# Kernel tuning notes

Hardware: AMD Instinct MI355X
Metric: run time of the kernel (lower is better)

Reference implementation:

```python
import jax, jax.numpy as jnp
import numpy as np

KEEP_FRAC = 0.8
HOP_CLIP = 15000  # reached hops are tiny; clip so score fits int32


def _bfs_keep_mask(src, dst, perm, n_nodes):
    """Replicates do_augmentation: BFS hop via u_add_e/min message passing,
    with a tie-break that seeds one unreached node when the frontier stalls,
    then keeps the 80% closest nodes (ties broken by perm)."""
    root = perm[0]
    w = jnp.where(src == dst, 0.0, 1.0).astype(jnp.float32)  # self-loop weight 0
    hop0 = jnp.full((n_nodes,), float(n_nodes), jnp.float32).at[root].set(0.0)
    thresh = n_nodes - 0.5
    cnt_target = int(n_nodes * KEEP_FRAC)

    def cond(state):
        return state[1] <= cnt_target

    def body(state):
        hop, cnt, hc = state
        m = jax.ops.segment_min(hop[src] + w, dst, num_segments=n_nodes)
        hop = jnp.minimum(m, hop)  # min-reduce (self-loops keep hop monotone)
        hc = hc + 1
        new_cnt = jnp.sum(hop < thresh).astype(jnp.int32)
        stuck = new_cnt == cnt
        # pick an unreached node (random in original; perm-ordered here)
        idx = jnp.argmin(jnp.where(hop > thresh, perm, 2 * n_nodes))
        hop = jnp.where(stuck, hop.at[idx].set(hc.astype(jnp.float32)), hop)
        new_cnt = new_cnt + stuck.astype(jnp.int32)
        return hop, new_cnt, hc

    cnt0 = jnp.sum(hop0 < thresh).astype(jnp.int32)
    hop, _, _ = jax.lax.while_loop(cond, body, (hop0, cnt0, jnp.int32(0)))
    score = jnp.minimum(hop, HOP_CLIP).astype(jnp.int32) * n_nodes + perm
    order = jnp.argsort(score)
    keep = jnp.zeros((n_nodes,), bool).at[order[:cnt_target]].set(True)
    return keep


def _gcn(x, src, dst, edge_mask, W_enc, n_nodes):
    # mean-aggregation GCN layer: h = relu(mean_{in-nbrs} x @ W)
    msg = x[src] * edge_mask[:, None]                      # [E, D]
    agg = jax.ops.segment_sum(msg, dst, num_segments=n_nodes)
    deg = jax.ops.segment_sum(edge_mask, dst, num_segments=n_nodes)
    return jax.nn.relu((agg / jnp.maximum(deg, 1.0)[:, None]) @ W_enc)


def _bce_with_logits(logits, positive):
    # BCEWithLogitsLoss: target=1 -> softplus(-x); target=0 -> softplus(x)
    return jnp.mean(jax.nn.softplus(jnp.where(positive, -logits, logits)))


def reference(feat, W_enc, W_disc, src, dst, perm_neg, perm1, perm2):
    n = feat.shape[0]
    ones_e = jnp.ones(src.shape[0], jnp.float32)
    pos = _gcn(feat, src, dst, ones_e, W_enc, n)           # [N, H]
    neg = _gcn(feat[perm_neg], src, dst, ones_e, W_enc, n)

    k = int(n * KEEP_FRAC)
    total = jnp.float32(0.0)
    for perm in (perm1, perm2):
        keep = _bfs_keep_mask(src, dst, perm, n)
        em = (keep[src] & keep[dst]).astype(jnp.float32)
        h = _gcn(feat * keep[:, None], src, dst, em, W_enc, n)
        summary = jax.nn.sigmoid(jnp.sum(h * keep[:, None], axis=0) / k)
        v = W_disc @ summary                               # [H]
        total = total + _bce_with_logits(pos @ v, True) + _bce_with_logits(neg @ v, False)
    return total


def setup_inputs() -> dict:
    key = jax.random.key(0)
    ks = jax.random.split(key, 8)
    N, D, H, DEG = 100000, 64, 64, 16
    E = N * DEG
    src = jnp.concatenate([jax.random.randint(ks[0], (E,), 0, N, jnp.int32),
                           jnp.arange(N, dtype=jnp.int32)])  # + self-loops
    dst = jnp.concatenate([jax.random.randint(ks[1], (E,), 0, N, jnp.int32),
                           jnp.arange(N, dtype=jnp.int32)])
    feat = jax.random.normal(ks[2], (N, D), jnp.float32)
    W_enc = jax.random.normal(ks[3], (D, H), jnp.float32) * (1.0 / np.sqrt(D))
    bound = 1.0 / np.sqrt(H)
    W_disc = jax.random.uniform(ks[4], (H, H), jnp.float32, -bound, bound)
    perm_neg = jax.random.permutation(ks[5], N).astype(jnp.int32)
    perm1 = jax.random.permutation(ks[6], N).astype(jnp.int32)
    perm2 = jax.random.permutation(ks[7], N).astype(jnp.int32)
    return {"feat": feat, "W_enc": W_enc, "W_disc": W_disc, "src": src,
            "dst": dst, "perm_neg": perm_neg, "perm1": perm1, "perm2": perm2}
```

## Files before the change

kernel.cpp:

```cpp
#include <hip/hip_runtime.h>
#include <hip/hip_fp8.h>
#include <hip/hip_fp16.h>

#define BS 256
#define MAXIT 7
#define UNREACHED 0x3f3f3f3f
#define NR 256
#define RB 256

#define C_DONE  0
#define C_CNT   1
#define C_BLKA  2
#define C_BLKB  3
#define C_BLKC  4
#define C_NEWA  20
#define C_LOSS  32
#define C_V1    192
#define C_V2    256

typedef __hip_fp8_e4m3 fp8;

#define ALr(p)   __hip_atomic_load((p), __ATOMIC_RELAXED, __HIP_MEMORY_SCOPE_AGENT)
#define ALf(p)   __hip_atomic_load((p), __ATOMIC_RELAXED, __HIP_MEMORY_SCOPE_AGENT)
#define ASr(p,v) __hip_atomic_store((p),(v), __ATOMIC_RELAXED, __HIP_MEMORY_SCOPE_AGENT)
#define ASl(p,v) __hip_atomic_store((p),(v), __ATOMIC_RELEASE, __HIP_MEMORY_SCOPE_AGENT)

__device__ inline float softplusf(float x){
  return fmaxf(x, 0.f) + log1pf(expf(-fabsf(x)));
}

__device__ inline void cut_hr(const int* __restrict__ ctl, int target, int& hstar, int& r){
  int c=1;
  hstar=63; r=0;
  for(int h=1;h<=MAXIT;h++){
    int x=ctl[C_NEWA+h-1];
    if(c+x>target){ hstar=h; r=target-c; return; }
    c+=x;
  }
  r=target-c;
}

__global__ void k_rhist(const int* __restrict__ dst, int E, int* __restrict__ hist,
                        int* __restrict__ bktBase, int nbk, int* __restrict__ ctrl){
  __shared__ int lh[512];
  int b=blockIdx.x, t=threadIdx.x;
  for(int i=t;i<nbk;i+=BS) lh[i]=0;
  __syncthreads();
  int per=(E+RB-1)/RB;
  int s0=b*per, s1=min(s0+per,E);
  for(int i=s0+t;i<s1;i+=BS) atomicAdd(&lh[dst[i]>>8],1);
  __syncthreads();
  for(int i=t;i<nbk;i+=BS) hist[i*RB+b]=lh[i];
  __shared__ int isLast;
  __syncthreads();
  if(t==0){
    __threadfence();
    isLast=(atomicAdd(&ctrl[C_BLKA],1)==(int)gridDim.x-1);
  }
  __syncthreads();
  if(!isLast) return;
  __threadfence();
  for(int r=t;r<nbk;r+=BS){
    const int* h=&hist[r*RB];
    int a=0;
    for(int bb=0;bb<RB;bb++) a+=ALr(&h[bb]);
    lh[r]=a;
  }
  __syncthreads();
  if(t==0){
    int acc=0;
    for(int r=0;r<nbk;r++){ bktBase[r]=acc; acc+=lh[r]; }
    bktBase[nbk]=E;
    ASr(&ctrl[C_BLKA],0);
    __threadfence();
  }
}

__global__ void k_cursors(const int* __restrict__ hist, const int* __restrict__ bktBase,
                          int* __restrict__ cursorTab, int nbk){
  __shared__ int s[BS];
  int r=blockIdx.x, t=threadIdx.x;
  if(r>=nbk) return;
  int v=hist[r*RB+t];
  s[t]=v; __syncthreads();
  for(int o=1;o<BS;o<<=1){
    int x=(t>=o)? s[t-o]:0;
    __syncthreads();
    if(t>=o) s[t]+=x;
    __syncthreads();
  }
  cursorTab[r*RB+t]=bktBase[r]+s[t]-v;
}

__global__ void k_rscatter(const int* __restrict__ dst, const int* __restrict__ src, int E,
                           const int* __restrict__ cursorTab,
                           unsigned long long* __restrict__ pairs, int nbk){
  __shared__ int cur[512];
  int b=blockIdx.x, t=threadIdx.x;
  for(int r=t;r<nbk;r+=BS) cur[r]=cursorTab[r*RB+b];
  __syncthreads();
  int per=(E+RB-1)/RB;
  int s0=b*per, s1=min(s0+per,E);
  for(int i=s0+t;i<s1;i+=BS){
    int d=dst[i], s=src[i];
    int pos=atomicAdd(&cur[d>>8],1);
    pairs[pos]=((unsigned long long)(unsigned)d<<32)|(unsigned)s;
  }
}

__global__ void k_bplace2(const int* __restrict__ bktBase, const unsigned long long* __restrict__ pairs,
                          int* __restrict__ rowptr, int* __restrict__ colD, int N, int E){
  __shared__ int cnt[NR];
  __shared__ int s[NR];
  __shared__ int cur[NR];
  int b=blockIdx.x, t=threadIdx.x;
  int v0=b*NR, v1=min(v0+NR,N), nv=v1-v0;
  int s0=bktBase[b], e0=bktBase[b+1];
  cnt[t]=0;
  __syncthreads();
  for(int i=s0+t;i<e0;i+=BS){
    int d=(int)(pairs[i]>>32);
    atomicAdd(&cnt[d-v0],1);
  }
  __syncthreads();
  int v=(t<nv)?cnt[t]:0;
  s[t]=v; __syncthreads();
  for(int o=1;o<BS;o<<=1){
    int x=(t>=o)? s[t-o]:0;
    __syncthreads();
    if(t>=o) s[t]+=x;
    __syncthreads();
  }
  int excl=s[t]-v+s0;
  if(t<nv){ rowptr[v0+t]=excl; cur[t]=excl; }
  if(b==0&&t==0) rowptr[N]=E;
  __syncthreads();
  for(int i=s0+t;i<e0;i+=BS){
    unsigned long long p=pairs[i];
    int d=(int)(p>>32), sv=(int)(p&0xffffffffu);
    int pos=atomicAdd(&cur[d-v0],1);
    colD[pos]=sv;
  }
}

__global__ void k_fw(const float* __restrict__ feat, const float* __restrict__ W,
                     fp8* __restrict__ FWI, int N){
  __shared__ float sW[64*64];
  __shared__ float sf[4][64];
  int t=threadIdx.x;
  for(int i=t;i<64*64;i+=BS) sW[i]=W[i];
  __syncthreads();
  int j=t&63, r=t>>6;
  int ngroups=(N+3)>>2;
  for(int g=blockIdx.x; g<ngroups; g+=gridDim.x){
    int vr=g*4+r;
    sf[r][j] = (vr<N)? feat[vr*64+j] : 0.f;
    __syncthreads();
    if(vr<N){
      float acc=0.f;
      #pragma unroll
      for(int d=0;d<64;d++) acc += sf[r][d]*sW[d*64+j];
      FWI[(size_t)vr*128+j]=fp8(acc);
    }
    __syncthreads();
  }
}

__global__ void k_permrows(unsigned* __restrict__ FWI, const int* __restrict__ pn, int N){
  int i=blockIdx.x*BS+threadIdx.x, st=gridDim.x*BS;
  int tot=N*16;
  for(; i<tot; i+=st){
    int v=i>>4, e=i&15;
    FWI[(size_t)v*32+16+e]=FWI[(size_t)pn[v]*32+e];
  }
}

__global__ void k_init2(int* __restrict__ hop1, int* __restrict__ hop2, int N,
                        const int* __restrict__ perm1, const int* __restrict__ perm2,
                        int* __restrict__ ctrl,
                        unsigned* __restrict__ bits1, unsigned* __restrict__ bits2,
                        int nw, int NB){
  int pb = blockIdx.x>=NB;
  int lb = blockIdx.x - (pb?NB:0);
  int* hop = pb? hop2:hop1;
  const int* perm = pb? perm2:perm1;
  unsigned* bits = pb? bits2:bits1;
  int* ctl = ctrl + pb*1024;
  int i=lb*BS+threadIdx.x, st=NB*BS;
  int root=perm[0];
  for(int v=i;v<N;v+=st) hop[v]=(v==root)?0:UNREACHED;
  for(int k=i;k<nw;k+=st) bits[k]=0u;
  if(lb==0&&threadIdx.x==0){
    ctl[C_DONE]=0; ctl[C_CNT]=1;
    ctl[C_BLKA]=0; ctl[C_BLKB]=0; ctl[C_BLKC]=0;
    for(int k=0;k<MAXIT;k++) ctl[C_NEWA+k]=0;
    if(!pb) ((float*)ctl)[C_LOSS]=0.f;
  }
}

__global__ void k_pull2(const int* __restrict__ rowptr, const int* __restrict__ col,
                        int* __restrict__ hop1, int* __restrict__ hop2,
                        const int* __restrict__ perm1, const int* __restrict__ perm2,
                        int* __restrict__ ctrl, int it, int N, int target, int NB){
  int pb = blockIdx.x>=NB;
  int lb = blockIdx.x - (pb?NB:0);
  int* hop = pb? hop2:hop1;
  const int* perm = pb? perm2:perm1;
  int* ctl = ctrl + pb*1024;
  if(ALr(&ctl[C_DONE])) return;
  int t=threadIdx.x;
  int lvl=it+1;
  int bn=0;
  for(int v=lb*BS+t; v<N; v+=NB*BS){
    if(hop[v]==UNREACHED){
      int b=rowptr[v], e=rowptr[v+1];
      for(int j=b;j<e;j++){
        int s=col[j];
        if(s==v) continue;
        if(hop[s]==lvl-1){ hop[v]=lvl; bn++; break; }
      }
    }
  }
  __shared__ int sred[BS];
  sred[t]=bn; __syncthreads();
  for(int o=BS/2;o>0;o>>=1){ if(t<o) sred[t]+=sred[t+o]; __syncthreads(); }
  __shared__ int isLast, totNew;
  if(t==0){
    if(sred[0]) atomicAdd(&ctl[C_NEWA+it], sred[0]);
    __threadfence();
    isLast=(atomicAdd(&ctl[C_BLKA],1)==NB-1);
  }
  __syncthreads();
  if(!isLast) return;
  __threadfence();
  if(t==0) totNew=ALr(&ctl[C_NEWA+it]);
  __syncthreads();
  int newly=totNew;
  __shared__ int seeded;
  if(newly==0){
    __shared__ unsigned long long sk[BS];
    unsigned long long key=~0ull;
    for(int v=t; v<N; v+=BS)
      if(ALr(&hop[v])==UNREACHED){
        unsigned long long k=((unsigned long long)(unsigned)perm[v]<<32)|(unsigned)v;
        if(k<key)key=k;
      }
    sk[t]=key; __syncthreads();
    for(int o=BS/2;o>0;o>>=1){ if(t<o&&sk[t+o]<sk[t])sk[t]=sk[t+o]; __syncthreads(); }
    if(t==0){
      seeded=0;
      if(sk[0]!=~0ull){
        int idx=(int)(sk[0]&0xffffffffu);
        ASr(&hop[idx],lvl);
        ctl[C_NEWA+it]=1;
        seeded=1;
      }
    }
    __syncthreads();
    newly=seeded;
  }
  if(t==0){
    int c=ctl[C_CNT]+newly;
    ctl[C_CNT]=c;
    if(c>target) ASl(&ctl[C_DONE],1);
    ASr(&ctl[C_BLKA],0);
    __threadfence();
  }
}

__global__ void k_flagscan2(const int* __restrict__ hop1, const int* __restrict__ hop2,
                            const int* __restrict__ perm1, const int* __restrict__ perm2,
                            unsigned* __restrict__ bits1, unsigned* __restrict__ bits2,
                            int* __restrict__ wordpref1, int* __restrict__ wordpref2,
                            int N, int nw, int* __restrict__ ctrl, int target, int NB){
  int pb = blockIdx.x>=NB;
  int lb = blockIdx.x - (pb?NB:0);
  const int* hop = pb? hop2:hop1;
  const int* perm = pb? perm2:perm1;
  unsigned* bits = pb? bits2:bits1;
  int* wordpref = pb? wordpref2:wordpref1;
  int* ctl = ctrl + pb*1024;
  int t=threadIdx.x;
  int hstar,rr; cut_hr(ctl,target,hstar,rr);
  for(int v=lb*BS+t; v<N; v+=NB*BS)
    if(min(hop[v],63)==hstar){
      int p=perm[v];
      atomicOr(&bits[p>>5], 1u<<(p&31));
    }
  __shared__ int isLast;
  if(t==0){
    __threadfence();
    isLast=(atomicAdd(&ctl[C_BLKC],1)==NB-1);
  }
  __syncthreads();
  if(!isLast) return;
  __threadfence();
  __shared__ int ss[BS];
  __shared__ int carry;
  if(t==0) carry=0;
  __syncthreads();
  for(int base=0; base<nw; base+=BS){
    int i=base+t;
    int v=(i<nw)? __popc(ALr(&bits[i])) : 0;
    ss[t]=v; __syncthreads();
    for(int o=1;o<BS;o<<=1){
      int x=(t>=o)? ss[t-o]:0;
      __syncthreads();
      if(t>=o) ss[t]+=x;
      __syncthreads();
    }
    if(i<nw) wordpref[i]=carry+ss[t]-v;
    __syncthreads();
    if(t==0) carry+=ss[BS-1];
    __syncthreads();
  }
  if(t==0){ ASr(&ctl[C_BLKC],0); __threadfence(); }
}

__global__ void k_keep2(const int* __restrict__ hop1, const int* __restrict__ hop2,
                        const int* __restrict__ perm1, const int* __restrict__ perm2,
                        const unsigned* __restrict__ bits1, const unsigned* __restrict__ bits2,
                        const int* __restrict__ wordpref1, const int* __restrict__ wordpref2,
                        int* __restrict__ keepPk, int N, const int* __restrict__ ctrl, int target){
  int h1,r1,h2,r2;
  cut_hr(ctrl,target,h1,r1);
  cut_hr(ctrl+1024,target,h2,r2);
  int i=blockIdx.x*BS+threadIdx.x, st=gridDim.x*BS;
  for(int v=i;v<N;v+=st){
    int h=min(hop1[v],63), kp1=0;
    if(h<h1) kp1=1;
    else if(h==h1){
      int p=perm1[v];
      unsigned mask=(2u<<(p&31))-1u;
      int cum=wordpref1[p>>5]+__popc(bits1[p>>5]&mask);
      kp1=(cum<=r1);
    }
    h=min(hop2[v],63); int kp2=0;
    if(h<h2) kp2=1;
    else if(h==h2){
      int p=perm2[v];
      unsigned mask=(2u<<(p&31))-1u;
      int cum=wordpref2[p>>5]+__popc(bits2[p>>5]&mask);
      kp2=(cum<=r2);
    }
    keepPk[v]=kp1|(kp2<<1);
  }
}

__global__ void __launch_bounds__(BS, 8) k_mega(
    const int* __restrict__ rowptr, const int* __restrict__ col,
    const unsigned char* __restrict__ FWI8, const int* __restrict__ keepPk,
    __half* __restrict__ P, __half* __restrict__ Q,
    float* __restrict__ sp1, float* __restrict__ sp2, int N){
  __shared__ uint4 lds4[4][8][8];
  __shared__ float sh1[4][64], sh2[4][64];
  int t=threadIdx.x, lane=t&63, w=t>>6;
  int eidx=lane>>3, q=lane&7;
  int woff=lane>>2, bsh=(lane&3)*8;
  volatile unsigned* l32=(volatile unsigned*)&lds4[w][0][0];
  int wid=(blockIdx.x*BS+t)>>6, nw=(gridDim.x*BS)>>6;
  float acc1=0.f, acc2=0.f;
  for(int v=wid; v<N; v+=nw){
    int b=rowptr[v], e=rowptr[v+1];
    int deg=e-b;
    int kv=keepPk[v];
    float ap=0.f, an=0.f, a1=0.f, a2=0.f;
    int c1t=0, c2t=0;
    for(int c0=b; c0<e; c0+=8){
      int n=min(8, e-c0);
      uint4 wa=make_uint4(0,0,0,0);
      int kk=0;
      if(eidx<n){
        int s=col[c0+eidx];
        if(q==0) kk=keepPk[s];
        wa=*reinterpret_cast<const uint4*>(FWI8+((size_t)s<<7)+(q<<4));
      }
      lds4[w][eidx][q]=wa;
      __asm__ volatile("" ::: "memory");
      unsigned long long bal1=__ballot(q==0 && (kk&1));
      unsigned long long bal2=__ballot(q==0 && (kk&2));
      c1t+=__popcll(bal1); c2t+=__popcll(bal2);
      if(n==8){
        #pragma unroll
        for(int ee=0; ee<8; ee++){
          unsigned ua=l32[ee*32+woff];
          unsigned ub=l32[ee*32+16+woff];
          fp8 ha, hb;
          ha.__x=(unsigned char)(ua>>bsh);
          hb.__x=(unsigned char)(ub>>bsh);
          float fa=(float)ha, fb=(float)hb;
          ap+=fa; an+=fb;
          a1 += ((bal1>>(ee*8))&1) ? fa : 0.f;
          a2 += ((bal2>>(ee*8))&1) ? fa : 0.f;
        }
      } else {
        for(int ee=0; ee<n; ee++){
          unsigned ua=l32[ee*32+woff];
          unsigned ub=l32[ee*32+16+woff];
          fp8 ha, hb;
          ha.__x=(unsigned char)(ua>>bsh);
          hb.__x=(unsigned char)(ub>>bsh);
          float fa=(float)ha, fb=(float)hb;
          ap+=fa; an+=fb;
          a1 += ((bal1>>(ee*8))&1) ? fa : 0.f;
          a2 += ((bal2>>(ee*8))&1) ? fa : 0.f;
        }
      }
      __asm__ volatile("" ::: "memory");
    }
    float invd=1.f/(float)deg;
    float p =fmaxf(ap*invd, 0.f);
    float qq=fmaxf(an*invd, 0.f);
    P[(size_t)v*64+lane]=__float2half(p);
    Q[(size_t)v*64+lane]=__float2half(qq);
    if(kv&1) acc1+=fmaxf(a1/(float)max(c1t,1), 0.f);
    if(kv&2) acc2+=fmaxf(a2/(float)max(c2t,1), 0.f);
  }
  sh1[w][lane]=acc1; sh2[w][lane]=acc2;
  __syncthreads();
  if(w==0){
    sp1[blockIdx.x*64+lane]=sh1[0][lane]+sh1[1][lane]+sh1[2][lane]+sh1[3][lane];
    sp2[blockIdx.x*64+lane]=sh2[0][lane]+sh2[1][lane]+sh2[2][lane]+sh2[3][lane];
  }
}

__global__ void k_redsum(const float* __restrict__ sp1, const float* __restrict__ sp2,
                         int nb, int rows, float* __restrict__ sp1b, float* __restrict__ sp2b,
                         const float* __restrict__ Wd, float* __restrict__ cf,
                         int* __restrict__ ctrl, float invk){
  __shared__ float s[BS];
  int t=threadIdx.x, lane=t&63, p=t>>6;
  int base=blockIdx.x*rows;
  float a=0.f;
  for(int r=p; r<rows; r+=4){ int row=base+r; if(row<nb) a+=sp1[row*64+lane]; }
  s[t]=a; __syncthreads();
  if(t<64) sp1b[blockIdx.x*64+t]=s[t]+s[t+64]+s[t+128]+s[t+192];
  __syncthreads();
  a=0.f;
  for(int r=p; r<rows; r+=4){ int row=base+r; if(row<nb) a+=sp2[row*64+lane]; }
  s[t]=a; __syncthreads();
  if(t<64) sp2b[blockIdx.x*64+t]=s[t]+s[t+64]+s[t+128]+s[t+192];
  __shared__ int isLast;
  __syncthreads();
  if(t==0){
    __threadfence();
    isLast=(atomicAdd(&ctrl[C_BLKB],1)==(int)gridDim.x-1);
  }
  __syncthreads();
  if(!isLast) return;
  __threadfence();
  int nb2=gridDim.x;
  __shared__ float sig[64];
  a=0.f;
  for(int b=p;b<nb2;b+=4) a+=ALf(&sp1b[b*64+lane]);
  s[t]=a; __syncthreads();
  if(t<64){
    float x=(s[t]+s[t+64]+s[t+128]+s[t+192])*invk;
    sig[t]=1.f/(1.f+expf(-x));
  }
  __syncthreads();
  if(t<64){
    float acc=0.f;
    #pragma unroll
    for(int d=0;d<64;d++) acc+=Wd[t*64+d]*sig[d];
    cf[C_V1+t]=acc;
  }
  __syncthreads();
  a=0.f;
  for(int b=p;b<nb2;b+=4) a+=ALf(&sp2b[b*64+lane]);
  s[t]=a; __syncthreads();
  if(t<64){
    float x=(s[t]+s[t+64]+s[t+128]+s[t+192])*invk;
    sig[t]=1.f/(1.f+expf(-x));
  }
  __syncthreads();
  if(t<64){
    float acc=0.f;
    #pragma unroll
    for(int d=0;d<64;d++) acc+=Wd[t*64+d]*sig[d];
    cf[C_V2+t]=acc;
  }
  if(t==0){ ASr(&ctrl[C_BLKB],0); __threadfence(); }
}

__global__ void k_loss2(const __half* __restrict__ P, const __half* __restrict__ Q,
                        float* __restrict__ cf, int* __restrict__ ctrl,
                        float* __restrict__ out, int N){
  __shared__ float sv1[64], sv2[64];
  __shared__ float sred[BS];
  int t=threadIdx.x;
  if(t<64){ sv1[t]=cf[C_V1+t]; sv2[t]=cf[C_V2+t]; }
  __syncthreads();
  int i=blockIdx.x*BS+t, st=gridDim.x*BS;
  float acc=0.f;
  for(int v=i; v<N; v+=st){
    const uint4* pr=(const uint4*)(P+(size_t)v*64);
    const uint4* qr=(const uint4*)(Q+(size_t)v*64);
    float a1=0.f,a2=0.f,b1=0.f,b2=0.f;
    #pragma unroll
    for(int c=0;c<8;c++){
      uint4 pu=pr[c], qu=qr[c];
      unsigned arr[4]={pu.x,pu.y,pu.z,pu.w};
      unsigned brr[4]={qu.x,qu.y,qu.z,qu.w};
      #pragma unroll
      for(int j=0;j<4;j++){
        int d=c*8+j*2;
        __half2 ph=*(const __half2*)&arr[j];
        __half2 qh=*(const __half2*)&brr[j];
        float2 pf=__half22float2(ph);
        float2 qf=__half22float2(qh);
        a1=fmaf(pf.x,sv1[d],a1); a1=fmaf(pf.y,sv1[d+1],a1);
        a2=fmaf(pf.x,sv2[d],a2); a2=fmaf(pf.y,sv2[d+1],a2);
        b1=fmaf(qf.x,sv1[d],b1); b1=fmaf(qf.y,sv1[d+1],b1);
        b2=fmaf(qf.x,sv2[d],b2); b2=fmaf(qf.y,sv2[d+1],b2);
      }
    }
    acc += softplusf(-a1)+softplusf(b1)+softplusf(-a2)+softplusf(b2);
  }
  sred[t]=acc;
  __syncthreads();
  for(int o=BS/2;o>0;o>>=1){ if(t<o) sred[t]+=sred[t+o]; __syncthreads(); }
  __shared__ int isLast;
  if(t==0){
    atomicAdd(&cf[C_LOSS], sred[0]);
    __threadfence();
    isLast=(atomicAdd(&ctrl[C_BLKC],1)==(int)gridDim.x-1);
  }
  __syncthreads();
  if(t==0 && isLast){
    __threadfence();
    out[0]=ALf(&cf[C_LOSS])/(float)N;
    ASr(&ctrl[C_BLKC],0);
  }
}

extern "C" void kernel_launch(void* const* d_in, const int* in_sizes, int n_in,
                              void* d_out, int out_size, void* d_ws, size_t ws_size,
                              hipStream_t stream) {
  const float* feat    = (const float*)d_in[0];
  const float* Wenc    = (const float*)d_in[1];
  const float* Wdisc   = (const float*)d_in[2];
  const int*   src     = (const int*)d_in[3];
  const int*   dst     = (const int*)d_in[4];
  const int*   permneg = (const int*)d_in[5];
  const int*   perm1   = (const int*)d_in[6];
  const int*   perm2   = (const int*)d_in[7];
  float* out = (float*)d_out;

  int N = in_sizes[5];
  int E = in_sizes[3];
  int target = (int)((double)N*0.8);
  int NB = (N+BS-1)/BS;
  int WORDS = (N+31)/32;
  int NBK = (N+NR-1)/NR;
  const int SUBB = 2048;
  const int R1B = 128, R1ROWS = SUBB/R1B;

  char* w = (char*)d_ws;
  auto alloc = [&](size_t bytes)->void*{
    void* p = (void*)w;
    w += (bytes + 255) & ~(size_t)255;
    return p;
  };
  int*      ctrl     = (int*)     alloc(8192);
  int*      rowptrD  = (int*)     alloc((size_t)(N+1)*4);
  int*      histD    = (int*)     alloc((size_t)RB*NBK*4);
  int*      cursorTab= (int*)     alloc((size_t)RB*NBK*4);
  int*      bktBase  = (int*)     alloc((size_t)(NBK+1)*4);
  int*      colD     = (int*)     alloc((size_t)E*4);
  unsigned long long* pairs = (unsigned long long*)alloc((size_t)E*8);
  int*      hop1     = (int*)     alloc((size_t)N*4);
  int*      hop2     = (int*)     alloc((size_t)N*4);
  int*      keepPk   = (int*)     alloc((size_t)N*4);
  unsigned* bits1    = (unsigned*)alloc((size_t)WORDS*4);
  unsigned* bits2    = (unsigned*)alloc((size_t)WORDS*4);
  int*      wordpref1= (int*)     alloc((size_t)(WORDS+1)*4);
  int*      wordpref2= (int*)     alloc((size_t)(WORDS+1)*4);
  fp8*      FWI      = (fp8*)     alloc((size_t)N*128);
  __half*   P        = (__half*)  alloc((size_t)N*64*2);
  __half*   Q        = (__half*)  alloc((size_t)N*64*2);
  float*    sp1      = (float*)   alloc((size_t)SUBB*64*4);
  float*    sp2      = (float*)   alloc((size_t)SUBB*64*4);
  float*    sp1b     = (float*)   alloc((size_t)R1B*64*4);
  float*    sp2b     = (float*)   alloc((size_t)R1B*64*4);
  float*    cf = (float*)ctrl;

  hipMemsetAsync(ctrl, 0, 8192, stream);

  k_rhist   <<<RB,  BS, 0, stream>>>(dst, E, histD, bktBase, NBK, ctrl);
  k_cursors <<<NBK, BS, 0, stream>>>(histD, bktBase, cursorTab, NBK);
  k_rscatter<<<RB,  BS, 0, stream>>>(dst, src, E, cursorTab, pairs, NBK);
  k_bplace2 <<<NBK, BS, 0, stream>>>(bktBase, pairs, rowptrD, colD, N, E);

  k_fw      <<<2048, BS, 0, stream>>>(feat, Wenc, FWI, N);
  k_permrows<<<4096, BS, 0, stream>>>((unsigned*)FWI, permneg, N);

  k_init2<<<2*NB, BS, 0, stream>>>(hop1, hop2, N, perm1, perm2, ctrl, bits1, bits2, WORDS, NB);
  for(int it=0; it<MAXIT; it++)
    k_pull2<<<2*NB, BS, 0, stream>>>(rowptrD, colD, hop1, hop2, perm1, perm2, ctrl, it, N, target, NB);
  k_flagscan2<<<2*NB, BS, 0, stream>>>(hop1, hop2, perm1, perm2, bits1, bits2,
                                       wordpref1, wordpref2, N, WORDS, ctrl, target, NB);
  k_keep2    <<<2*NB, BS, 0, stream>>>(hop1, hop2, perm1, perm2, bits1, bits2,
                                       wordpref1, wordpref2, keepPk, N, ctrl, target);

  k_mega  <<<SUBB, BS, 0, stream>>>(rowptrD, colD, (const unsigned char*)FWI, keepPk,
                                    P, Q, sp1, sp2, N);
  k_redsum<<<R1B, BS, 0, stream>>>(sp1, sp2, SUBB, R1ROWS, sp1b, sp2b, Wdisc, cf, ctrl,
                                   1.f/(float)target);

  k_loss2<<<NB, BS, 0, stream>>>(P, Q, cf, ctrl, out, N);
}
```

Baseline: 547.5 us.

## Use edge-parallel push BFS with frontier bitmap for early levels; pack scatter pairs

The first five BFS levels now use a new edge-parallel push kernel over the raw src/dst arrays. It filters edges through a visited bitmap plus the previous hop level and claims newly reached nodes with atomicCAS. Later levels still use the CSR pull kernel. Separately, the radix-scatter pairs shrink from 64-bit to 32-bit by storing only the low 8 bits of dst within its bucket next to a 24-bit src. This halves the traffic of the CSR build. The push kernel scans all E edges every level, and the 24-bit packing assumes N stays below 16M.

```diff
diff --git a/kernel.cpp b/kernel.cpp
--- a/kernel.cpp
+++ b/kernel.cpp
@@ -94,7 +94,7 @@
 
 __global__ void k_rscatter(const int* __restrict__ dst, const int* __restrict__ src, int E,
                            const int* __restrict__ cursorTab,
-                           unsigned long long* __restrict__ pairs, int nbk){
+                           unsigned* __restrict__ pairs, int nbk){
   __shared__ int cur[512];
   int b=blockIdx.x, t=threadIdx.x;
   for(int r=t;r<nbk;r+=BS) cur[r]=cursorTab[r*RB+b];
@@ -104,11 +104,11 @@
   for(int i=s0+t;i<s1;i+=BS){
     int d=dst[i], s=src[i];
     int pos=atomicAdd(&cur[d>>8],1);
-    pairs[pos]=((unsigned long long)(unsigned)d<<32)|(unsigned)s;
-  }
-}
-
-__global__ void k_bplace2(const int* __restrict__ bktBase, const unsigned long long* __restrict__ pairs,
+    pairs[pos]=((unsigned)(d&255)<<24)|(unsigned)s;
+  }
+}
+
+__global__ void k_bplace2(const int* __restrict__ bktBase, const unsigned* __restrict__ pairs,
                           int* __restrict__ rowptr, int* __restrict__ colD, int N, int E){
   __shared__ int cnt[NR];
   __shared__ int s[NR];
@@ -119,8 +119,7 @@
   cnt[t]=0;
   __syncthreads();
   for(int i=s0+t;i<e0;i+=BS){
-    int d=(int)(pairs[i]>>32);
-    atomicAdd(&cnt[d-v0],1);
+    atomicAdd(&cnt[pairs[i]>>24],1);
   }
   __syncthreads();
   int v=(t<nv)?cnt[t]:0;
@@ -136,10 +135,9 @@
   if(b==0&&t==0) rowptr[N]=E;
   __syncthreads();
   for(int i=s0+t;i<e0;i+=BS){
-    unsigned long long p=pairs[i];
-    int d=(int)(p>>32), sv=(int)(p&0xffffffffu);
-    int pos=atomicAdd(&cur[d-v0],1);
-    colD[pos]=sv;
+    unsigned pr=pairs[i];
+    int pos=atomicAdd(&cur[pr>>24],1);
+    colD[pos]=(int)(pr&0xFFFFFFu);
   }
 }
 
@@ -178,23 +176,101 @@
 __global__ void k_init2(int* __restrict__ hop1, int* __restrict__ hop2, int N,
                         const int* __restrict__ perm1, const int* __restrict__ perm2,
                         int* __restrict__ ctrl,
+                        unsigned* __restrict__ bmap1, unsigned* __restrict__ bmap2,
                         unsigned* __restrict__ bits1, unsigned* __restrict__ bits2,
                         int nw, int NB){
   int pb = blockIdx.x>=NB;
   int lb = blockIdx.x - (pb?NB:0);
   int* hop = pb? hop2:hop1;
   const int* perm = pb? perm2:perm1;
+  unsigned* bmap = pb? bmap2:bmap1;
   unsigned* bits = pb? bits2:bits1;
   int* ctl = ctrl + pb*1024;
   int i=lb*BS+threadIdx.x, st=NB*BS;
   int root=perm[0];
+  int rw=root>>5; unsigned rbit=1u<<(root&31);
   for(int v=i;v<N;v+=st) hop[v]=(v==root)?0:UNREACHED;
-  for(int k=i;k<nw;k+=st) bits[k]=0u;
+  for(int k=i;k<nw;k+=st){ bmap[k]=(k==rw)?rbit:0u; bits[k]=0u; }
   if(lb==0&&threadIdx.x==0){
     ctl[C_DONE]=0; ctl[C_CNT]=1;
     ctl[C_BLKA]=0; ctl[C_BLKB]=0; ctl[C_BLKC]=0;
     for(int k=0;k<MAXIT;k++) ctl[C_NEWA+k]=0;
     if(!pb) ((float*)ctl)[C_LOSS]=0.f;
+  }
+}
+
+__global__ void k_epush2(const int* __restrict__ src, const int* __restrict__ dst, int E,
+                         int* __restrict__ hop1, int* __restrict__ hop2,
+                         unsigned* __restrict__ bmap1, unsigned* __restrict__ bmap2,
+                         const int* __restrict__ perm1, const int* __restrict__ perm2,
+                         int* __restrict__ ctrl, int it, int N, int target, int EB){
+  int pb = blockIdx.x>=EB;
+  int lb = blockIdx.x - (pb?EB:0);
+  int* hop = pb? hop2:hop1;
+  unsigned* bmap = pb? bmap2:bmap1;
+  const int* perm = pb? perm2:perm1;
+  int* ctl = ctrl + pb*1024;
+  if(ALr(&ctl[C_DONE])) return;
+  int t=threadIdx.x;
+  int lvl=it+1, prev=it;
+  int updB=(it<4);
+  int bn=0;
+  for(int e=lb*BS+t; e<E; e+=EB*BS){
+    int s=src[e];
+    if(!((bmap[s>>5]>>(s&31))&1u)) continue;
+    if(hop[s]!=prev) continue;
+    int d=dst[e];
+    if(d==s) continue;
+    if(hop[d]==UNREACHED && atomicCAS(&hop[d],UNREACHED,lvl)==UNREACHED){
+      if(updB) atomicOr(&bmap[d>>5],1u<<(d&31));
+      bn++;
+    }
+  }
+  __shared__ int sred[BS];
+  sred[t]=bn; __syncthreads();
+  for(int o=BS/2;o>0;o>>=1){ if(t<o) sred[t]+=sred[t+o]; __syncthreads(); }
+  __shared__ int isLast, totNew;
+  if(t==0){
+    if(sred[0]) atomicAdd(&ctl[C_NEWA+it], sred[0]);
+    __threadfence();
+    isLast=(atomicAdd(&ctl[C_BLKA],1)==EB-1);
+  }
+  __syncthreads();
+  if(!isLast) return;
+  __threadfence();
+  if(t==0) totNew=ALr(&ctl[C_NEWA+it]);
+  __syncthreads();
+  int newly=totNew;
+  __shared__ int seeded;
+  if(newly==0){
+    __shared__ unsigned long long sk[BS];
+    unsigned long long key=~0ull;
+    for(int v=t; v<N; v+=BS)
+      if(ALr(&hop[v])==UNREACHED){
+        unsigned long long k=((unsigned long long)(unsigned)perm[v]<<32)|(unsigned)v;
+        if(k<key)key=k;
+      }
+    sk[t]=key; __syncthreads();
+    for(int o=BS/2;o>0;o>>=1){ if(t<o&&sk[t+o]<sk[t])sk[t]=sk[t+o]; __syncthreads(); }
+    if(t==0){
+      seeded=0;
+      if(sk[0]!=~0ull){
+        int idx=(int)(sk[0]&0xffffffffu);
+        ASr(&hop[idx],lvl);
+        if(updB) atomicOr(&bmap[idx>>5],1u<<(idx&31));
+        ctl[C_NEWA+it]=1;
+        seeded=1;
+      }
+    }
+    __syncthreads();
+    newly=seeded;
+  }
+  if(t==0){
+    int c=ctl[C_CNT]+newly;
+    ctl[C_CNT]=c;
+    if(c>target) ASl(&ctl[C_DONE],1);
+    ASr(&ctl[C_BLKA],0);
+    __threadfence();
   }
 }
 
@@ -555,6 +631,8 @@
   int NBK = (N+NR-1)/NR;
   const int SUBB = 2048;
   const int R1B = 128, R1ROWS = SUBB/R1B;
+  const int EB = 512;
+  const int EPUSH_LVLS = 5;
 
   char* w = (char*)d_ws;
   auto alloc = [&](size_t bytes)->void*{
@@ -568,10 +646,12 @@
   int*      cursorTab= (int*)     alloc((size_t)RB*NBK*4);
   int*      bktBase  = (int*)     alloc((size_t)(NBK+1)*4);
   int*      colD     = (int*)     alloc((size_t)E*4);
-  unsigned long long* pairs = (unsigned long long*)alloc((size_t)E*8);
+  unsigned* pairs    = (unsigned*)alloc((size_t)E*4);
   int*      hop1     = (int*)     alloc((size_t)N*4);
   int*      hop2     = (int*)     alloc((size_t)N*4);
   int*      keepPk   = (int*)     alloc((size_t)N*4);
+  unsigned* bmap1    = (unsigned*)alloc((size_t)WORDS*4);
+  unsigned* bmap2    = (unsigned*)alloc((size_t)WORDS*4);
   unsigned* bits1    = (unsigned*)alloc((size_t)WORDS*4);
   unsigned* bits2    = (unsigned*)alloc((size_t)WORDS*4);
   int*      wordpref1= (int*)     alloc((size_t)(WORDS+1)*4);
@@ -595,9 +675,16 @@
   k_fw      <<<2048, BS, 0, stream>>>(feat, Wenc, FWI, N);
   k_permrows<<<4096, BS, 0, stream>>>((unsigned*)FWI, permneg, N);
 
-  k_init2<<<2*NB, BS, 0, stream>>>(hop1, hop2, N, perm1, perm2, ctrl, bits1, bits2, WORDS, NB);
-  for(int it=0; it<MAXIT; it++)
-    k_pull2<<<2*NB, BS, 0, stream>>>(rowptrD, colD, hop1, hop2, perm1, perm2, ctrl, it, N, target, NB);
+  k_init2<<<2*NB, BS, 0, stream>>>(hop1, hop2, N, perm1, perm2, ctrl, bmap1, bmap2,
+                                   bits1, bits2, WORDS, NB);
+  for(int it=0; it<MAXIT; it++){
+    if(it<EPUSH_LVLS)
+      k_epush2<<<2*EB, BS, 0, stream>>>(src, dst, E, hop1, hop2, bmap1, bmap2,
+                                        perm1, perm2, ctrl, it, N, target, EB);
+    else
+      k_pull2<<<2*NB, BS, 0, stream>>>(rowptrD, colD, hop1, hop2, perm1, perm2,
+                                       ctrl, it, N, target, NB);
+  }
   k_flagscan2<<<2*NB, BS, 0, stream>>>(hop1, hop2, perm1, perm2, bits1, bits2,
                                        wordpref1, wordpref2, N, WORDS, ctrl, target, NB);
   k_keep2    <<<2*NB, BS, 0, stream>>>(hop1, hop2, perm1, perm2, bits1, bits2,
```

Result: slower. 646.5 us (+18.1%).

## Fuse the two BFS pull passes over shared CSR and pack edge pairs to 32 bits

Applied to the files above, without the earlier changes.

The two independent BFS traversals (perm1 and perm2) now run in one pull kernel with a single grid, so each unreached vertex's CSR row is read once and checked against both hop arrays. The early break only happens once both searches have found a parent. Separately, the bucket-scatter pairs buffer shrinks from 64-bit to 32-bit words: the local destination index (d&255) goes in the top 8 bits and the source in the low 24 bits. Both changes cut memory traffic, but the packing assumes N fits in 24 bits, and the fused loop can scan longer rows when only one search still needs a parent.

```diff
diff --git a/kernel.cpp b/kernel.cpp
--- a/kernel.cpp
+++ b/kernel.cpp
@@ -94,7 +94,7 @@
 
 __global__ void k_rscatter(const int* __restrict__ dst, const int* __restrict__ src, int E,
                            const int* __restrict__ cursorTab,
-                           unsigned long long* __restrict__ pairs, int nbk){
+                           unsigned* __restrict__ pairs, int nbk){
   __shared__ int cur[512];
   int b=blockIdx.x, t=threadIdx.x;
   for(int r=t;r<nbk;r+=BS) cur[r]=cursorTab[r*RB+b];
@@ -104,11 +104,11 @@
   for(int i=s0+t;i<s1;i+=BS){
     int d=dst[i], s=src[i];
     int pos=atomicAdd(&cur[d>>8],1);
-    pairs[pos]=((unsigned long long)(unsigned)d<<32)|(unsigned)s;
-  }
-}
-
-__global__ void k_bplace2(const int* __restrict__ bktBase, const unsigned long long* __restrict__ pairs,
+    pairs[pos]=((unsigned)(d&255)<<24)|(unsigned)s;
+  }
+}
+
+__global__ void k_bplace2(const int* __restrict__ bktBase, const unsigned* __restrict__ pairs,
                           int* __restrict__ rowptr, int* __restrict__ colD, int N, int E){
   __shared__ int cnt[NR];
   __shared__ int s[NR];
@@ -119,8 +119,7 @@
   cnt[t]=0;
   __syncthreads();
   for(int i=s0+t;i<e0;i+=BS){
-    int d=(int)(pairs[i]>>32);
-    atomicAdd(&cnt[d-v0],1);
+    atomicAdd(&cnt[pairs[i]>>24],1);
   }
   __syncthreads();
   int v=(t<nv)?cnt[t]:0;
@@ -136,10 +135,9 @@
   if(b==0&&t==0) rowptr[N]=E;
   __syncthreads();
   for(int i=s0+t;i<e0;i+=BS){
-    unsigned long long p=pairs[i];
-    int d=(int)(p>>32), sv=(int)(p&0xffffffffu);
-    int pos=atomicAdd(&cur[d-v0],1);
-    colD[pos]=sv;
+    unsigned pr=pairs[i];
+    int pos=atomicAdd(&cur[pr>>24],1);
+    colD[pos]=(int)(pr&0xFFFFFFu);
   }
 }
 
@@ -198,73 +196,124 @@
   }
 }
 
-__global__ void k_pull2(const int* __restrict__ rowptr, const int* __restrict__ col,
+__global__ void k_pullF(const int* __restrict__ rowptr, const int* __restrict__ col,
                         int* __restrict__ hop1, int* __restrict__ hop2,
                         const int* __restrict__ perm1, const int* __restrict__ perm2,
-                        int* __restrict__ ctrl, int it, int N, int target, int NB){
-  int pb = blockIdx.x>=NB;
-  int lb = blockIdx.x - (pb?NB:0);
-  int* hop = pb? hop2:hop1;
-  const int* perm = pb? perm2:perm1;
-  int* ctl = ctrl + pb*1024;
-  if(ALr(&ctl[C_DONE])) return;
+                        int* __restrict__ ctrl, int it, int N, int target){
   int t=threadIdx.x;
   int lvl=it+1;
-  int bn=0;
-  for(int v=lb*BS+t; v<N; v+=NB*BS){
-    if(hop[v]==UNREACHED){
-      int b=rowptr[v], e=rowptr[v+1];
-      for(int j=b;j<e;j++){
-        int s=col[j];
-        if(s==v) continue;
-        if(hop[s]==lvl-1){ hop[v]=lvl; bn++; break; }
+  int done1=ALr(&ctrl[C_DONE]);
+  int done2=ALr(&ctrl[1024+C_DONE]);
+  if(done1&&done2) return;
+  int bn1=0, bn2=0;
+  for(int v=blockIdx.x*BS+t; v<N; v+=gridDim.x*BS){
+    bool u1=(!done1)&&(hop1[v]==UNREACHED);
+    bool u2=(!done2)&&(hop2[v]==UNREACHED);
+    if(!(u1||u2)) continue;
+    int b=rowptr[v], e=rowptr[v+1];
+    for(int j=b;j<e;j++){
+      int s=col[j];
+      if(s==v) continue;
+      if(u1 && hop1[s]==lvl-1){ hop1[v]=lvl; bn1++; u1=false; }
+      if(u2 && hop2[s]==lvl-1){ hop2[v]=lvl; bn2++; u2=false; }
+      if(!(u1||u2)) break;
+    }
+  }
+  __shared__ int sred[BS];
+  __shared__ unsigned long long sk[BS];
+  if(!done1){
+    sred[t]=bn1; __syncthreads();
+    for(int o=BS/2;o>0;o>>=1){ if(t<o) sred[t]+=sred[t+o]; __syncthreads(); }
+    __shared__ int isLast1, totNew1;
+    if(t==0){
+      if(sred[0]) atomicAdd(&ctrl[C_NEWA+it], sred[0]);
+      __threadfence();
+      isLast1=(atomicAdd(&ctrl[C_BLKA],1)==(int)gridDim.x-1);
+    }
+    __syncthreads();
+    if(isLast1){
+      __threadfence();
+      if(t==0) totNew1=ALr(&ctrl[C_NEWA+it]);
+      __syncthreads();
+      int newly=totNew1;
+      __shared__ int seeded1;
+      if(newly==0){
+        unsigned long long key=~0ull;
+        for(int v=t; v<N; v+=BS)
+          if(ALr(&hop1[v])==UNREACHED){
+            unsigned long long k=((unsigned long long)(unsigned)perm1[v]<<32)|(unsigned)v;
+            if(k<key)key=k;
+          }
+        sk[t]=key; __syncthreads();
+        for(int o=BS/2;o>0;o>>=1){ if(t<o&&sk[t+o]<sk[t])sk[t]=sk[t+o]; __syncthreads(); }
+        if(t==0){
+          seeded1=0;
+          if(sk[0]!=~0ull){
+            int idx=(int)(sk[0]&0xffffffffu);
+            ASr(&hop1[idx],lvl);
+            ctrl[C_NEWA+it]=1;
+            seeded1=1;
+          }
+        }
+        __syncthreads();
+        newly=seeded1;
       }
-    }
-  }
-  __shared__ int sred[BS];
-  sred[t]=bn; __syncthreads();
-  for(int o=BS/2;o>0;o>>=1){ if(t<o) sred[t]+=sred[t+o]; __syncthreads(); }
-  __shared__ int isLast, totNew;
-  if(t==0){
-    if(sred[0]) atomicAdd(&ctl[C_NEWA+it], sred[0]);
-    __threadfence();
-    isLast=(atomicAdd(&ctl[C_BLKA],1)==NB-1);
-  }
-  __syncthreads();
-  if(!isLast) return;
-  __threadfence();
-  if(t==0) totNew=ALr(&ctl[C_NEWA+it]);
-  __syncthreads();
-  int newly=totNew;
-  __shared__ int seeded;
-  if(newly==0){
-    __shared__ unsigned long long sk[BS];
-    unsigned long long key=~0ull;
-    for(int v=t; v<N; v+=BS)
-      if(ALr(&hop[v])==UNREACHED){
-        unsigned long long k=((unsigned long long)(unsigned)perm[v]<<32)|(unsigned)v;
-        if(k<key)key=k;
+      if(t==0){
+        int c=ctrl[C_CNT]+newly;
+        ctrl[C_CNT]=c;
+        if(c>target) ASl(&ctrl[C_DONE],1);
+        ASr(&ctrl[C_BLKA],0);
+        __threadfence();
       }
-    sk[t]=key; __syncthreads();
-    for(int o=BS/2;o>0;o>>=1){ if(t<o&&sk[t+o]<sk[t])sk[t]=sk[t+o]; __syncthreads(); }
+    }
+    __syncthreads();
+  }
+  if(!done2){
+    int* ctl=ctrl+1024;
+    sred[t]=bn2; __syncthreads();
+    for(int o=BS/2;o>0;o>>=1){ if(t<o) sred[t]+=sred[t+o]; __syncthreads(); }
+    __shared__ int isLast2, totNew2;
     if(t==0){
-      seeded=0;
-      if(sk[0]!=~0ull){
-        int idx=(int)(sk[0]&0xffffffffu);
-        ASr(&hop[idx],lvl);
-        ctl[C_NEWA+it]=1;
-        seeded=1;
+      if(sred[0]) atomicAdd(&ctl[C_NEWA+it], sred[0]);
+      __threadfence();
+      isLast2=(atomicAdd(&ctl[C_BLKA],1)==(int)gridDim.x-1);
+    }
+    __syncthreads();
+    if(isLast2){
+      __threadfence();
+      if(t==0) totNew2=ALr(&ctl[C_NEWA+it]);
+      __syncthreads();
+      int newly=totNew2;
+      __shared__ int seeded2;
+      if(newly==0){
+        unsigned long long key=~0ull;
+        for(int v=t; v<N; v+=BS)
+          if(ALr(&hop2[v])==UNREACHED){
+            unsigned long long k=((unsigned long long)(unsigned)perm2[v]<<32)|(unsigned)v;
+            if(k<key)key=k;
+          }
+        sk[t]=key; __syncthreads();
+        for(int o=BS/2;o>0;o>>=1){ if(t<o&&sk[t+o]<sk[t])sk[t]=sk[t+o]; __syncthreads(); }
+        if(t==0){
+          seeded2=0;
+          if(sk[0]!=~0ull){
+            int idx=(int)(sk[0]&0xffffffffu);
+            ASr(&hop2[idx],lvl);
+            ctl[C_NEWA+it]=1;
+            seeded2=1;
+          }
+        }
+        __syncthreads();
+        newly=seeded2;
       }
-    }
-    __syncthreads();
-    newly=seeded;
-  }
-  if(t==0){
-    int c=ctl[C_CNT]+newly;
-    ctl[C_CNT]=c;
-    if(c>target) ASl(&ctl[C_DONE],1);
-    ASr(&ctl[C_BLKA],0);
-    __threadfence();
+      if(t==0){
+        int c=ctl[C_CNT]+newly;
+        ctl[C_CNT]=c;
+        if(c>target) ASl(&ctl[C_DONE],1);
+        ASr(&ctl[C_BLKA],0);
+        __threadfence();
+      }
+    }
   }
 }
 
@@ -568,7 +617,7 @@
   int*      cursorTab= (int*)     alloc((size_t)RB*NBK*4);
   int*      bktBase  = (int*)     alloc((size_t)(NBK+1)*4);
   int*      colD     = (int*)     alloc((size_t)E*4);
-  unsigned long long* pairs = (unsigned long long*)alloc((size_t)E*8);
+  unsigned* pairs    = (unsigned*)alloc((size_t)E*4);
   int*      hop1     = (int*)     alloc((size_t)N*4);
   int*      hop2     = (int*)     alloc((size_t)N*4);
   int*      keepPk   = (int*)     alloc((size_t)N*4);
@@ -597,7 +646,7 @@
 
   k_init2<<<2*NB, BS, 0, stream>>>(hop1, hop2, N, perm1, perm2, ctrl, bits1, bits2, WORDS, NB);
   for(int it=0; it<MAXIT; it++)
-    k_pull2<<<2*NB, BS, 0, stream>>>(rowptrD, colD, hop1, hop2, perm1, perm2, ctrl, it, N, target, NB);
+    k_pullF<<<NB, BS, 0, stream>>>(rowptrD, colD, hop1, hop2, perm1, perm2, ctrl, it, N, target);
   k_flagscan2<<<2*NB, BS, 0, stream>>>(hop1, hop2, perm1, perm2, bits1, bits2,
                                        wordpref1, wordpref2, N, WORDS, ctrl, target, NB);
   k_keep2    <<<2*NB, BS, 0, stream>>>(hop1, hop2, perm1, perm2, bits1, bits2,
```

After: 538.2 us. Within noise of the previous version (-1.7%).
